# Kernel optimization log

Measured on AMD Instinct MI355X. Metric: run time of the kernel, lower is better.

The kernel has to match this reference:

```python
import jax, jax.numpy as jnp
import numpy as np

EMBED_DIM = 1024
NUM_HEADS = 16
HEAD_DIM = EMBED_DIM // NUM_HEADS
B, S = 2, 2048


def _xavier(k, shape):
    # xavier_uniform for square [out,in] weight
    limit = float(np.sqrt(6.0 / (shape[0] + shape[1])))
    return jax.random.uniform(k, shape, jnp.float32, -limit, limit)


def setup_inputs() -> dict:
    key = jax.random.key(0)
    ks = jax.random.split(key, 7)
    return {
        "query": jax.random.normal(ks[0], (B, S, EMBED_DIM), jnp.float32),
        "key": jax.random.normal(ks[1], (B, S, EMBED_DIM), jnp.float32),
        "value": jax.random.normal(ks[2], (B, S, EMBED_DIM), jnp.float32),
        "Wq": _xavier(ks[3], (EMBED_DIM, EMBED_DIM)),
        "Wk": _xavier(ks[4], (EMBED_DIM, EMBED_DIM)),
        "Wv": _xavier(ks[5], (EMBED_DIM, EMBED_DIM)),
        "Wo": _xavier(ks[6], (EMBED_DIM, EMBED_DIM)),
    }


def _orthogonalize(Wq, Wk):
    # Both projections computed from the ORIGINAL weights, then both replaced
    # (matches torch: weight1_proj/weight2_proj computed before copy_).
    Wq_o = Wq - Wq @ (Wk.T @ Wk)
    Wk_o = Wk - Wk @ (Wq.T @ Wq)
    return Wq_o, Wk_o


def reference(query, key, value, Wq, Wk, Wv, Wo):
    Wq_o, Wk_o = _orthogonalize(Wq, Wk)
    # F.linear(x, W) = x @ W.T
    q = query @ Wq_o.T
    k = key @ Wk_o.T
    v = value @ Wv.T
    # [B, S, E] -> [B, H, S, Dh]
    def split_heads(x):
        return x.reshape(B, -1, NUM_HEADS, HEAD_DIM).transpose(0, 2, 1, 3)
    q, k, v = split_heads(q), split_heads(k), split_heads(v)
    scale = 1.0 / (HEAD_DIM ** 0.5)
    scores = jnp.einsum("bhqd,bhkd->bhqk", q, k) * scale
    attn = jax.nn.softmax(scores, axis=-1)
    out = jnp.einsum("bhqk,bhkd->bhqd", attn, v)
    out = out.transpose(0, 2, 1, 3).reshape(B, -1, EMBED_DIM)
    return out @ Wo.T
```

## Files before the change

### kernel.cpp

```cpp
#include <hip/hip_runtime.h>
#include <math.h>

constexpr int EMBED  = 1024;
constexpr int NHEADS = 16;
constexpr int HDIM   = 64;
constexpr int BATCH  = 2;
constexpr int SEQ    = 2048;
constexpr int MROWS  = BATCH * SEQ;

typedef unsigned short u16b;
typedef __attribute__((ext_vector_type(8))) short bfrag;
typedef __attribute__((ext_vector_type(4))) float ffrag;
typedef __attribute__((ext_vector_type(16))) float f16frag;
typedef __attribute__((ext_vector_type(4))) int i32x4;

#define SCALE_Q 0.18033688f

__device__ __forceinline__ u16b f2b(float f) {
    union { float f; unsigned u; } v; v.f = f;
    unsigned r = v.u + 0x7fffu + ((v.u >> 16) & 1u);
    return (u16b)(r >> 16);
}

__device__ __forceinline__ unsigned cvtpk_bf16(float a, float b) {
    unsigned r;
    asm("v_cvt_pk_bf16_f32 %0, %1, %2" : "=v"(r) : "v"(a), "v"(b));
    return r;
}

__device__ __forceinline__ void plane_swap(unsigned a, unsigned b, int& lo, int& hi) {
    auto r = __builtin_amdgcn_permlane32_swap((int)a, (int)b, false, false);
    lo = (int)r[0];
    hi = (int)r[1];
}

__device__ __forceinline__ void gload_lds16(const u16b* g, u16b* l) {
    __builtin_amdgcn_global_load_lds(
        (const __attribute__((address_space(1))) void*)g,
        (__attribute__((address_space(3))) void*)l,
        16, 0, 0);
}

struct GemmPtrs {
    const u16b* A[3];
    const u16b* B[3];
    const float* D[3];
    u16b* Cb[3];
    float* Cf[3];
    float scale[3];
    int vt[3];
    int hs[3];
};

__global__ void prep_all(const float* __restrict__ q, const float* __restrict__ k,
                         const float* __restrict__ v,
                         const float* __restrict__ Wq, const float* __restrict__ Wk,
                         const float* __restrict__ Wv, const float* __restrict__ Wo,
                         u16b* __restrict__ oq, u16b* __restrict__ ok, u16b* __restrict__ ov,
                         u16b* __restrict__ wq, u16b* __restrict__ wk,
                         u16b* __restrict__ wv, u16b* __restrict__ wo,
                         u16b* __restrict__ wqt, u16b* __restrict__ wkt) {
    const int z = blockIdx.z;
    const int tid = threadIdx.x;
    if (z < 3) {
        const float* src = (z == 0) ? q : (z == 1) ? k : v;
        u16b* dst = (z == 0) ? oq : (z == 1) ? ok : ov;
        const int i = blockIdx.x * 256 + tid;
        float4 val = ((const float4*)src)[i];
        ushort4 o;
        o.x = f2b(val.x); o.y = f2b(val.y); o.z = f2b(val.z); o.w = f2b(val.w);
        ((ushort4*)dst)[i] = o;
        return;
    }
    if (blockIdx.x >= 1024) return;
    const int w = z - 3;
    const float* src = (w == 0) ? Wq : (w == 1) ? Wk : (w == 2) ? Wv : Wo;
    u16b* dst  = (w == 0) ? wq : (w == 1) ? wk : (w == 2) ? wv : wo;
    u16b* dstT = (w == 0) ? wqt : (w == 1) ? wkt : nullptr;
    __shared__ float t[32][33];
    const int bx = (blockIdx.x & 31) * 32, by = (blockIdx.x >> 5) * 32;
    const int x = tid & 31, y = tid >> 5;
#pragma unroll
    for (int r = 0; r < 4; ++r) {
        const int row = by + y + 8 * r;
        const float val = src[(size_t)row * EMBED + bx + x];
        dst[(size_t)row * EMBED + bx + x] = f2b(val);
        if (w < 2) t[y + 8 * r][x] = val;
    }
    if (w >= 2) return;
    __syncthreads();
#pragma unroll
    for (int r = 0; r < 4; ++r)
        dstT[(size_t)(bx + y + 8 * r) * EMBED + by + x] = f2b(t[x][y + 8 * r]);
}

template<int MODE>
__global__ __launch_bounds__(256) void gemm64(GemmPtrs p, int M, int N, int K) {
    const int z = blockIdx.z;
    const u16b* __restrict__ A = p.A[z];
    const u16b* __restrict__ B = p.B[z];
    const float* __restrict__ D = p.D[z];
    u16b* __restrict__ Cb = p.Cb[z];
    const float scale = p.scale[z];

    __shared__ __align__(16) u16b As[64 * 32];
    __shared__ __align__(16) u16b Bs[64 * 32];

    const int tid = threadIdx.x;
    const int wave = tid >> 6, lane = tid & 63;
    const int quad = lane >> 4, l16 = lane & 15;
    const int wrow = wave >> 1, wcol = wave & 1;
    const int m0 = blockIdx.y * 64, n0 = blockIdx.x * 64;

    ffrag acc[2][2];
#pragma unroll
    for (int i = 0; i < 2; ++i)
#pragma unroll
        for (int j = 0; j < 2; ++j) acc[i][j] = ffrag{0.f, 0.f, 0.f, 0.f};

    const int srow = tid >> 2, schunk = tid & 3;

    for (int kt = 0; kt < K; kt += 32) {
        gload_lds16(A + (size_t)(m0 + srow) * K + kt + schunk * 8, &As[wave * 512]);
        gload_lds16(B + (size_t)(n0 + srow) * K + kt + schunk * 8, &Bs[wave * 512]);
        __syncthreads();
        bfrag a[2], bv[2];
#pragma unroll
        for (int i = 0; i < 2; ++i)
            a[i] = *(const bfrag*)&As[(wrow * 32 + i * 16 + l16) * 32 + quad * 8];
#pragma unroll
        for (int j = 0; j < 2; ++j)
            bv[j] = *(const bfrag*)&Bs[(wcol * 32 + j * 16 + l16) * 32 + quad * 8];
#pragma unroll
        for (int i = 0; i < 2; ++i)
#pragma unroll
            for (int j = 0; j < 2; ++j)
                acc[i][j] = __builtin_amdgcn_mfma_f32_16x16x32_bf16(a[i], bv[j], acc[i][j], 0, 0, 0);
        __syncthreads();
    }

#pragma unroll
    for (int i = 0; i < 2; ++i)
#pragma unroll
        for (int j = 0; j < 2; ++j) {
            const int col = n0 + wcol * 32 + j * 16 + l16;
#pragma unroll
            for (int r = 0; r < 4; ++r) {
                const int row = m0 + wrow * 32 + i * 16 + quad * 4 + r;
                const size_t idx = (size_t)row * N + col;
                const float v = acc[i][j][r];
                if (MODE == 0) Cb[idx] = f2b(v * scale);
                else Cb[idx] = f2b(D[idx] - v);
            }
        }
}

template<int MODE, int BM>
__global__ __launch_bounds__(256) void gemm_big(GemmPtrs p, int M, int N, int K) {
    const int z = blockIdx.z;
    const u16b* __restrict__ A = p.A[z];
    const u16b* __restrict__ B = p.B[z];
    u16b* __restrict__ Cb = p.Cb[z];
    float* __restrict__ Cf = p.Cf[z];
    const float scale = p.scale[z];
    const int vt = p.vt[z], hs = p.hs[z];

    constexpr int BK = 32;
    constexpr int IT = BM / 32;
    constexpr int IA = BM / 64;
    __shared__ __align__(16) u16b As[BM * BK];
    __shared__ __align__(16) u16b Bs[128 * BK];

    const int tid = threadIdx.x;
    const int wave = tid >> 6, lane = tid & 63;
    const int quad = lane >> 4, l16 = lane & 15;
    const int wrow = wave >> 1, wcol = wave & 1;
    const int m0 = blockIdx.y * BM, n0 = blockIdx.x * 128;

    ffrag acc[IT][4];
#pragma unroll
    for (int i = 0; i < IT; ++i)
#pragma unroll
        for (int j = 0; j < 4; ++j) acc[i][j] = ffrag{0.f, 0.f, 0.f, 0.f};

    const int srow = lane >> 2, schunk = lane & 3;

    for (int kt = 0; kt < K; kt += BK) {
#pragma unroll
        for (int q = 0; q < IA; ++q) {
            int row = wave * (BM / 4) + q * 16;
            gload_lds16(A + (size_t)(m0 + row + srow) * K + kt + schunk * 8, &As[row * BK]);
        }
#pragma unroll
        for (int q = 0; q < 2; ++q) {
            int row = wave * 32 + q * 16;
            gload_lds16(B + (size_t)(n0 + row + srow) * K + kt + schunk * 8, &Bs[row * BK]);
        }
        __syncthreads();
        bfrag af[IT], bfv[4];
#pragma unroll
        for (int i = 0; i < IT; ++i)
            af[i] = *(const bfrag*)&As[(wrow * (BM / 2) + i * 16 + l16) * BK + quad * 8];
#pragma unroll
        for (int j = 0; j < 4; ++j)
            bfv[j] = *(const bfrag*)&Bs[(wcol * 64 + j * 16 + l16) * BK + quad * 8];
#pragma unroll
        for (int i = 0; i < IT; ++i)
#pragma unroll
            for (int j = 0; j < 4; ++j)
                acc[i][j] = __builtin_amdgcn_mfma_f32_16x16x32_bf16(af[i], bfv[j], acc[i][j], 0, 0, 0);
        __syncthreads();
    }

    if (MODE == 0 && vt) {
#pragma unroll
        for (int i = 0; i < IT; ++i)
#pragma unroll
            for (int j = 0; j < 4; ++j) {
                const int col = n0 + wcol * 64 + j * 16 + l16;
                const int h = col >> 6, d = col & 63;
                const int row0 = m0 + wrow * (BM / 2) + i * 16 + quad * 4;
                const int b = row0 >> 11, s = row0 & 2047;
                ushort4 o;
                o.x = f2b(acc[i][j][0]); o.y = f2b(acc[i][j][1]);
                o.z = f2b(acc[i][j][2]); o.w = f2b(acc[i][j][3]);
                *(ushort4*)&Cb[((size_t)(b * NHEADS + h) * HDIM + d) * SEQ + s] = o;
            }
        return;
    }
    if (MODE == 0 && hs) {
#pragma unroll
        for (int i = 0; i < IT; ++i)
#pragma unroll
            for (int j = 0; j < 4; ++j) {
                const int col = n0 + wcol * 64 + j * 16 + l16;
                const int h = col >> 6, d = col & 63;
                const int row0 = m0 + wrow * (BM / 2) + i * 16 + quad * 4;
                const int b = row0 >> 11, s0 = row0 & 2047;
#pragma unroll
                for (int r = 0; r < 4; ++r)
                    Cb[((size_t)(b * NHEADS + h) * SEQ + s0 + r) * HDIM + d] =
                        f2b(acc[i][j][r] * scale);
            }
        return;
    }

#pragma unroll
    for (int i = 0; i < IT; ++i)
#pragma unroll
        for (int j = 0; j < 4; ++j) {
            const int col = n0 + wcol * 64 + j * 16 + l16;
#pragma unroll
            for (int r = 0; r < 4; ++r) {
                const int row = m0 + wrow * (BM / 2) + i * 16 + quad * 4 + r;
                const size_t idx = (size_t)row * N + col;
                const float v = acc[i][j][r];
                if (MODE == 0) Cb[idx] = f2b(v * scale);
                else Cf[idx] = v;
            }
        }
}

__global__ __launch_bounds__(256) void flash_attn6(
    const u16b* __restrict__ Qp, const u16b* __restrict__ Kp,
    const u16b* __restrict__ Vt, float* __restrict__ Opart,
    float* __restrict__ Lpart)
{
    const int tid = threadIdx.x;
    const int wave = tid >> 6, lane = tid & 63;
    const int l32 = lane & 31, hi = lane >> 5;
    const int qt = blockIdx.x, h = blockIdx.y;
    const int b = blockIdx.z >> 1, sp = blockIdx.z & 1;
    const int qb = qt * 128 + wave * 32;
    const int kt0 = sp * (SEQ / 2), kt1 = kt0 + SEQ / 2;

    __shared__ __align__(16) u16b Ks[2][64 * 64];
    __shared__ __align__(16) u16b Vs[2][64 * 64];

    const size_t hsbase = (size_t)(b * NHEADS + h) * SEQ;
    const size_t vtbase = (size_t)(b * NHEADS + h) * HDIM * SEQ;
    const size_t obase  = ((size_t)sp * MROWS + (size_t)b * SEQ) * EMBED + h * HDIM;

    bfrag bq[4];
#pragma unroll
    for (int ks = 0; ks < 4; ++ks)
        bq[ks] = *(const bfrag*)&Qp[(hsbase + qb + l32) * HDIM + ks * 16 + hi * 8];

    f16frag ov0, ov1;
#pragma unroll
    for (int r = 0; r < 16; ++r) { ov0[r] = 0.f; ov1[r] = 0.f; }
    float l_run = 0.f;

    const int r0 = tid >> 3, c0 = tid & 7;
    const int sw0 = (r0 * 8 + (c0 ^ (r0 & 7))) * 8;
    const int sw1 = ((r0 + 32) * 8 + (c0 ^ (r0 & 7))) * 8;
    const u16b* kgb = Kp + hsbase * HDIM;
    const u16b* vgb = Vt + vtbase;

    {
        const u16b* kg = kgb + (size_t)kt0 * HDIM;
        bfrag k0 = *(const bfrag*)(kg + tid * 8);
        bfrag k1 = *(const bfrag*)(kg + (tid + 256) * 8);
        bfrag v0 = *(const bfrag*)(vgb + (size_t)r0 * SEQ + kt0 + c0 * 8);
        bfrag v1 = *(const bfrag*)(vgb + (size_t)(r0 + 32) * SEQ + kt0 + c0 * 8);
        *(bfrag*)&Ks[0][sw0] = k0;  *(bfrag*)&Ks[0][sw1] = k1;
        *(bfrag*)&Vs[0][sw0] = v0;  *(bfrag*)&Vs[0][sw1] = v1;
    }
    __syncthreads();

    int p = 0;
    for (int kt = kt0; kt < kt1; kt += 64, p ^= 1) {
        const bool more = (kt + 64) < kt1;
        bfrag kn0, kn1, vn0, vn1;
        if (more) {
            const u16b* kg = kgb + (size_t)(kt + 64) * HDIM;
            kn0 = *(const bfrag*)(kg + tid * 8);
            kn1 = *(const bfrag*)(kg + (tid + 256) * 8);
            vn0 = *(const bfrag*)(vgb + (size_t)r0 * SEQ + kt + 64 + c0 * 8);
            vn1 = *(const bfrag*)(vgb + (size_t)(r0 + 32) * SEQ + kt + 64 + c0 * 8);
        }

        f16frag St0, St1;
#pragma unroll
        for (int r = 0; r < 16; ++r) { St0[r] = 0.f; St1[r] = 0.f; }
#pragma unroll
        for (int ks = 0; ks < 4; ++ks) {
            const int ch = ks * 2 + hi;
            bfrag k0 = *(const bfrag*)&Ks[p][(l32 * 8 + (ch ^ (l32 & 7))) * 8];
            bfrag k1 = *(const bfrag*)&Ks[p][((32 + l32) * 8 + (ch ^ (l32 & 7))) * 8];
            St0 = __builtin_amdgcn_mfma_f32_32x32x16_bf16(k0, bq[ks], St0, 0, 0, 0);
            St1 = __builtin_amdgcn_mfma_f32_32x32x16_bf16(k1, bq[ks], St1, 0, 0, 0);
        }

        float rs = 0.f;
#pragma unroll
        for (int r = 0; r < 16; ++r) {
            const float a = __builtin_amdgcn_exp2f(St0[r]);
            const float c = __builtin_amdgcn_exp2f(St1[r]);
            St0[r] = a; St1[r] = c;
            rs += a + c;
        }
        rs += __shfl_xor(rs, 32);
        l_run += rs;

        unsigned d0[8], d1[8];
#pragma unroll
        for (int rr = 0; rr < 8; ++rr) {
            d0[rr] = cvtpk_bf16(St0[2 * rr], St0[2 * rr + 1]);
            d1[rr] = cvtpk_bf16(St1[2 * rr], St1[2 * rr + 1]);
        }
        bfrag bp[4];
        {
            int a0, a1, b0, b1, c0w, c1, e0, e1;
            plane_swap(d0[0], d0[2], a0, a1);
            plane_swap(d0[1], d0[3], b0, b1);
            i32x4 w = { a0, b0, a1, b1 };
            bp[0] = __builtin_bit_cast(bfrag, w);
            plane_swap(d0[4], d0[6], c0w, c1);
            plane_swap(d0[5], d0[7], e0, e1);
            i32x4 w2 = { c0w, e0, c1, e1 };
            bp[1] = __builtin_bit_cast(bfrag, w2);
        }
        {
            int a0, a1, b0, b1, c0w, c1, e0, e1;
            plane_swap(d1[0], d1[2], a0, a1);
            plane_swap(d1[1], d1[3], b0, b1);
            i32x4 w = { a0, b0, a1, b1 };
            bp[2] = __builtin_bit_cast(bfrag, w);
            plane_swap(d1[4], d1[6], c0w, c1);
            plane_swap(d1[5], d1[7], e0, e1);
            i32x4 w2 = { c0w, e0, c1, e1 };
            bp[3] = __builtin_bit_cast(bfrag, w2);
        }

#pragma unroll
        for (int ks = 0; ks < 4; ++ks) {
            const int ch = ks * 2 + hi;
            bfrag v0 = *(const bfrag*)&Vs[p][(l32 * 8 + (ch ^ (l32 & 7))) * 8];
            bfrag v1 = *(const bfrag*)&Vs[p][((32 + l32) * 8 + (ch ^ (l32 & 7))) * 8];
            ov0 = __builtin_amdgcn_mfma_f32_32x32x16_bf16(v0, bp[ks], ov0, 0, 0, 0);
            ov1 = __builtin_amdgcn_mfma_f32_32x32x16_bf16(v1, bp[ks], ov1, 0, 0, 0);
        }

        if (more) {
            *(bfrag*)&Ks[p ^ 1][sw0] = kn0;  *(bfrag*)&Ks[p ^ 1][sw1] = kn1;
            *(bfrag*)&Vs[p ^ 1][sw0] = vn0;  *(bfrag*)&Vs[p ^ 1][sw1] = vn1;
            __syncthreads();
        }
    }

    const size_t orow = obase + (size_t)(qb + l32) * EMBED;
#pragma unroll
    for (int rr = 0; rr < 4; ++rr) {
        float4 o0, o1;
        o0.x = ov0[4 * rr + 0]; o0.y = ov0[4 * rr + 1];
        o0.z = ov0[4 * rr + 2]; o0.w = ov0[4 * rr + 3];
        o1.x = ov1[4 * rr + 0]; o1.y = ov1[4 * rr + 1];
        o1.z = ov1[4 * rr + 2]; o1.w = ov1[4 * rr + 3];
        *(float4*)&Opart[orow + rr * 8 + hi * 4] = o0;
        *(float4*)&Opart[orow + 32 + rr * 8 + hi * 4] = o1;
    }
    if (hi == 0)
        Lpart[((size_t)sp * BATCH * NHEADS + b * NHEADS + h) * SEQ + qb + l32] = l_run;
}

__global__ void combine_o(const float* __restrict__ O0, const float* __restrict__ O1,
                          const float* __restrict__ L0, const float* __restrict__ L1,
                          u16b* __restrict__ ao) {
    const int i = blockIdx.x * 256 + threadIdx.x;
    const int e0 = i << 2;
    const int row = e0 >> 10, col = e0 & 1023;
    const int lidx = ((row >> 11) * NHEADS + (col >> 6)) * SEQ + (row & 2047);
    float4 a = ((const float4*)O0)[i];
    float4 c = ((const float4*)O1)[i];
    const float inv = 1.f / (L0[lidx] + L1[lidx]);
    ushort4 o;
    o.x = f2b((a.x + c.x) * inv); o.y = f2b((a.y + c.y) * inv);
    o.z = f2b((a.z + c.z) * inv); o.w = f2b((a.w + c.w) * inv);
    ((ushort4*)ao)[i] = o;
}

extern "C" void kernel_launch(void* const* d_in, const int* in_sizes, int n_in,
                              void* d_out, int out_size, void* d_ws, size_t ws_size,
                              hipStream_t stream) {
    const float* query = (const float*)d_in[0];
    const float* key_  = (const float*)d_in[1];
    const float* value = (const float*)d_in[2];
    const float* Wq    = (const float*)d_in[3];
    const float* Wk    = (const float*)d_in[4];
    const float* Wv    = (const float*)d_in[5];
    const float* Wo    = (const float*)d_in[6];
    float* out = (float*)d_out;

    char* ws = (char*)d_ws;
    const size_t MB = 1024 * 1024;
    u16b* xq  = (u16b*)(ws + 0 * MB);
    u16b* xk  = (u16b*)(ws + 8 * MB);
    u16b* xv  = (u16b*)(ws + 16 * MB);
    u16b* wq  = (u16b*)(ws + 24 * MB);
    u16b* wk  = (u16b*)(ws + 26 * MB);
    u16b* wv  = (u16b*)(ws + 28 * MB);
    u16b* gq  = (u16b*)(ws + 32 * MB);
    u16b* gk  = (u16b*)(ws + 34 * MB);
    u16b* wqo = (u16b*)(ws + 36 * MB);
    u16b* wko = (u16b*)(ws + 38 * MB);
    u16b* wo  = (u16b*)(ws + 40 * MB);
    u16b* qp  = (u16b*)(ws + 44 * MB);
    u16b* kp  = (u16b*)(ws + 52 * MB);
    u16b* Vt  = (u16b*)(ws + 60 * MB);
    u16b* wqt = (u16b*)(ws + 60 * MB);
    u16b* wkt = (u16b*)(ws + 62 * MB);
    float* Op  = (float*)(ws + 0 * MB);
    float* Lp  = (float*)(ws + 32 * MB);
    u16b*  ao  = (u16b*)(ws + 44 * MB);

    prep_all<<<dim3(MROWS * EMBED / 1024, 1, 7), dim3(256), 0, stream>>>(
        query, key_, value, Wq, Wk, Wv, Wo,
        xq, xk, xv, wq, wk, wv, wo, wqt, wkt);

    {
        GemmPtrs p{};
        p.A[0] = wqt; p.B[0] = wqt; p.Cb[0] = gq; p.scale[0] = 1.f;
        p.A[1] = wkt; p.B[1] = wkt; p.Cb[1] = gk; p.scale[1] = 1.f;
        gemm64<0><<<dim3(16, 16, 2), dim3(256), 0, stream>>>(p, EMBED, EMBED, EMBED);
    }
    {
        GemmPtrs p{};
        p.A[0] = wq; p.B[0] = gk; p.D[0] = Wq; p.Cb[0] = wqo;
        p.A[1] = wk; p.B[1] = gq; p.D[1] = Wk; p.Cb[1] = wko;
        gemm64<1><<<dim3(16, 16, 2), dim3(256), 0, stream>>>(p, EMBED, EMBED, EMBED);
    }
    {
        GemmPtrs p{};
        p.A[0] = xq; p.B[0] = wqo; p.Cb[0] = qp; p.scale[0] = SCALE_Q; p.hs[0] = 1;
        p.A[1] = xk; p.B[1] = wko; p.Cb[1] = kp; p.scale[1] = 1.f;     p.hs[1] = 1;
        p.A[2] = xv; p.B[2] = wv;  p.Cb[2] = Vt; p.scale[2] = 1.f;     p.vt[2] = 1;
        gemm_big<0, 128><<<dim3(EMBED / 128, MROWS / 128, 3), dim3(256), 0, stream>>>(
            p, MROWS, EMBED, EMBED);
    }
    flash_attn6<<<dim3(SEQ / 128, NHEADS, BATCH * 2), dim3(256), 0, stream>>>(
        qp, kp, Vt, Op, Lp);
    combine_o<<<dim3(MROWS * EMBED / 1024), dim3(256), 0, stream>>>(
        Op, Op + (size_t)MROWS * EMBED, Lp, Lp + (size_t)BATCH * NHEADS * SEQ, ao);
    {
        GemmPtrs p{};
        p.A[0] = ao; p.B[0] = wo; p.Cf[0] = out; p.scale[0] = 1.f;
        gemm_big<2, 64><<<dim3(EMBED / 128, MROWS / 64, 1), dim3(256), 0, stream>>>(
            p, MROWS, EMBED, EMBED);
    }
}
```

Before: 293.3 us.

## Double-buffer LDS staging in gemm_big and use it for weight GEMMs

Gives gemm_big two LDS buffers so the global-to-LDS copy of the next K-tile is issued before the MFMAs on the current tile, overlapping load latency with compute. It also removes the separate 64x64 gemm64 kernel. The two weight-orthogonalisation GEMMs now run through gemm_big with BM=64, and a MODE==1 epilogue computes D-v for them. In exchange, LDS use per block doubles, which may lower occupancy, and the weight GEMMs launch fewer, larger blocks.

```diff
diff --git a/kernel.cpp b/kernel.cpp
--- a/kernel.cpp
+++ b/kernel.cpp
@@ -94,73 +94,13 @@
         dstT[(size_t)(bx + y + 8 * r) * EMBED + by + x] = f2b(t[x][y + 8 * r]);
 }
 
-template<int MODE>
-__global__ __launch_bounds__(256) void gemm64(GemmPtrs p, int M, int N, int K) {
+template<int MODE, int BM>
+__global__ __launch_bounds__(256) void gemm_big(GemmPtrs p, int M, int N, int K) {
     const int z = blockIdx.z;
     const u16b* __restrict__ A = p.A[z];
     const u16b* __restrict__ B = p.B[z];
     const float* __restrict__ D = p.D[z];
     u16b* __restrict__ Cb = p.Cb[z];
-    const float scale = p.scale[z];
-
-    __shared__ __align__(16) u16b As[64 * 32];
-    __shared__ __align__(16) u16b Bs[64 * 32];
-
-    const int tid = threadIdx.x;
-    const int wave = tid >> 6, lane = tid & 63;
-    const int quad = lane >> 4, l16 = lane & 15;
-    const int wrow = wave >> 1, wcol = wave & 1;
-    const int m0 = blockIdx.y * 64, n0 = blockIdx.x * 64;
-
-    ffrag acc[2][2];
-#pragma unroll
-    for (int i = 0; i < 2; ++i)
-#pragma unroll
-        for (int j = 0; j < 2; ++j) acc[i][j] = ffrag{0.f, 0.f, 0.f, 0.f};
-
-    const int srow = tid >> 2, schunk = tid & 3;
-
-    for (int kt = 0; kt < K; kt += 32) {
-        gload_lds16(A + (size_t)(m0 + srow) * K + kt + schunk * 8, &As[wave * 512]);
-        gload_lds16(B + (size_t)(n0 + srow) * K + kt + schunk * 8, &Bs[wave * 512]);
-        __syncthreads();
-        bfrag a[2], bv[2];
-#pragma unroll
-        for (int i = 0; i < 2; ++i)
-            a[i] = *(const bfrag*)&As[(wrow * 32 + i * 16 + l16) * 32 + quad * 8];
-#pragma unroll
-        for (int j = 0; j < 2; ++j)
-            bv[j] = *(const bfrag*)&Bs[(wcol * 32 + j * 16 + l16) * 32 + quad * 8];
-#pragma unroll
-        for (int i = 0; i < 2; ++i)
-#pragma unroll
-            for (int j = 0; j < 2; ++j)
-                acc[i][j] = __builtin_amdgcn_mfma_f32_16x16x32_bf16(a[i], bv[j], acc[i][j], 0, 0, 0);
-        __syncthreads();
-    }
-
-#pragma unroll
-    for (int i = 0; i < 2; ++i)
-#pragma unroll
-        for (int j = 0; j < 2; ++j) {
-            const int col = n0 + wcol * 32 + j * 16 + l16;
-#pragma unroll
-            for (int r = 0; r < 4; ++r) {
-                const int row = m0 + wrow * 32 + i * 16 + quad * 4 + r;
-                const size_t idx = (size_t)row * N + col;
-                const float v = acc[i][j][r];
-                if (MODE == 0) Cb[idx] = f2b(v * scale);
-                else Cb[idx] = f2b(D[idx] - v);
-            }
-        }
-}
-
-template<int MODE, int BM>
-__global__ __launch_bounds__(256) void gemm_big(GemmPtrs p, int M, int N, int K) {
-    const int z = blockIdx.z;
-    const u16b* __restrict__ A = p.A[z];
-    const u16b* __restrict__ B = p.B[z];
-    u16b* __restrict__ Cb = p.Cb[z];
     float* __restrict__ Cf = p.Cf[z];
     const float scale = p.scale[z];
     const int vt = p.vt[z], hs = p.hs[z];
@@ -168,8 +108,8 @@
     constexpr int BK = 32;
     constexpr int IT = BM / 32;
     constexpr int IA = BM / 64;
-    __shared__ __align__(16) u16b As[BM * BK];
-    __shared__ __align__(16) u16b Bs[128 * BK];
+    __shared__ __align__(16) u16b As[2][BM * BK];
+    __shared__ __align__(16) u16b Bs[2][128 * BK];
 
     const int tid = threadIdx.x;
     const int wave = tid >> 6, lane = tid & 63;
@@ -185,25 +125,34 @@
 
     const int srow = lane >> 2, schunk = lane & 3;
 
-    for (int kt = 0; kt < K; kt += BK) {
+    auto STAGE = [&](int buf, int kt) {
 #pragma unroll
         for (int q = 0; q < IA; ++q) {
             int row = wave * (BM / 4) + q * 16;
-            gload_lds16(A + (size_t)(m0 + row + srow) * K + kt + schunk * 8, &As[row * BK]);
+            gload_lds16(A + (size_t)(m0 + row + srow) * K + kt + schunk * 8,
+                        &As[buf][row * BK]);
         }
 #pragma unroll
         for (int q = 0; q < 2; ++q) {
             int row = wave * 32 + q * 16;
-            gload_lds16(B + (size_t)(n0 + row + srow) * K + kt + schunk * 8, &Bs[row * BK]);
-        }
-        __syncthreads();
+            gload_lds16(B + (size_t)(n0 + row + srow) * K + kt + schunk * 8,
+                        &Bs[buf][row * BK]);
+        }
+    };
+
+    STAGE(0, 0);
+    __syncthreads();
+
+    int cur = 0;
+    for (int kt = 0; kt < K; kt += BK, cur ^= 1) {
+        if (kt + BK < K) STAGE(cur ^ 1, kt + BK);
         bfrag af[IT], bfv[4];
 #pragma unroll
         for (int i = 0; i < IT; ++i)
-            af[i] = *(const bfrag*)&As[(wrow * (BM / 2) + i * 16 + l16) * BK + quad * 8];
+            af[i] = *(const bfrag*)&As[cur][(wrow * (BM / 2) + i * 16 + l16) * BK + quad * 8];
 #pragma unroll
         for (int j = 0; j < 4; ++j)
-            bfv[j] = *(const bfrag*)&Bs[(wcol * 64 + j * 16 + l16) * BK + quad * 8];
+            bfv[j] = *(const bfrag*)&Bs[cur][(wcol * 64 + j * 16 + l16) * BK + quad * 8];
 #pragma unroll
         for (int i = 0; i < IT; ++i)
 #pragma unroll
@@ -256,6 +205,7 @@
                 const size_t idx = (size_t)row * N + col;
                 const float v = acc[i][j][r];
                 if (MODE == 0) Cb[idx] = f2b(v * scale);
+                else if (MODE == 1) Cb[idx] = f2b(D[idx] - v);
                 else Cf[idx] = v;
             }
         }
@@ -462,13 +412,15 @@
         GemmPtrs p{};
         p.A[0] = wqt; p.B[0] = wqt; p.Cb[0] = gq; p.scale[0] = 1.f;
         p.A[1] = wkt; p.B[1] = wkt; p.Cb[1] = gk; p.scale[1] = 1.f;
-        gemm64<0><<<dim3(16, 16, 2), dim3(256), 0, stream>>>(p, EMBED, EMBED, EMBED);
+        gemm_big<0, 64><<<dim3(EMBED / 128, EMBED / 64, 2), dim3(256), 0, stream>>>(
+            p, EMBED, EMBED, EMBED);
     }
     {
         GemmPtrs p{};
         p.A[0] = wq; p.B[0] = gk; p.D[0] = Wq; p.Cb[0] = wqo;
         p.A[1] = wk; p.B[1] = gq; p.D[1] = Wk; p.Cb[1] = wko;
-        gemm64<1><<<dim3(16, 16, 2), dim3(256), 0, stream>>>(p, EMBED, EMBED, EMBED);
+        gemm_big<1, 64><<<dim3(EMBED / 128, EMBED / 64, 2), dim3(256), 0, stream>>>(
+            p, EMBED, EMBED, EMBED);
     }
     {
         GemmPtrs p{};
```

Result: faster. 284.7 us (-2.9%).
